# Performance work log

Hardware: AMD Instinct MI355X
Metric: run time of the kernel (lower is better)

The kernel has to match this reference:

```python
import jax, jax.numpy as jnp
import numpy as np

B, S, E, H = 2, 4096, 512, 8
DK = E // H


def setup_inputs() -> dict:
    k = jax.random.key(0)
    ks = jax.random.split(k, 11)
    sc = 0.02
    return {
        "query": jax.random.normal(ks[0], (B, S, E), jnp.float32),
        "key_in": jax.random.normal(ks[1], (B, S, E), jnp.float32),
        "value": jax.random.normal(ks[2], (B, S, E), jnp.float32),
        "Wq": jax.random.normal(ks[3], (E, E), jnp.float32) * sc,
        "bq": jax.random.normal(ks[4], (E,), jnp.float32) * sc,
        "Wk": jax.random.normal(ks[5], (E, E), jnp.float32) * sc,
        "bk": jax.random.normal(ks[6], (E,), jnp.float32) * sc,
        "Wv": jax.random.normal(ks[7], (E, E), jnp.float32) * sc,
        "bv": jax.random.normal(ks[8], (E,), jnp.float32) * sc,
        "Wo": jax.random.normal(ks[9], (E, E), jnp.float32) * sc,
        "bo": jax.random.normal(ks[10], (E,), jnp.float32) * sc,
    }


def reference(query, key_in, value, Wq, bq, Wk, bk, Wv, bv, Wo, bo):
    b, s, _ = query.shape
    # Linear projections
    q = query @ Wq + bq
    k = key_in @ Wk + bk
    v = value @ Wv + bv
    # [b, s, H, dk] -> [b, H, s, dk]
    q = q.reshape(b, s, H, DK).transpose(0, 2, 1, 3)
    k = k.reshape(b, s, H, DK).transpose(0, 2, 1, 3)
    v = v.reshape(b, s, H, DK).transpose(0, 2, 1, 3)
    # NOTE: source bug — softmax over UNSCALED scores (1/sqrt scaling in the
    # original is applied to a dead variable after softmax). Reproduce faithfully.
    scores = jnp.einsum("bhqd,bhkd->bhqk", q, k)  # [b,H,s,s] — O(N^2) materialized
    weights = jax.nn.softmax(scores.astype(jnp.float32), axis=-1)
    attn = jnp.einsum("bhqk,bhkd->bhqd", weights, v)
    # [b,H,s,dk] -> [b,s,E]
    concat = attn.transpose(0, 2, 1, 3).reshape(b, s, E)
    return concat @ Wo + bo
```

## Files before the change

### kernel.cpp

```cpp
#include <hip/hip_runtime.h>
#include <hip/hip_bf16.h>

#define B_  2
#define S_  4096
#define E_  512
#define H_  8
#define DK_ 64
#define M_  8192

typedef float f32x4  __attribute__((ext_vector_type(4)));
typedef float f32x16 __attribute__((ext_vector_type(16)));
typedef short s16x8  __attribute__((ext_vector_type(8)));
typedef short s16x4  __attribute__((ext_vector_type(4)));

static __device__ __forceinline__ short f2bf(float x) {
  __hip_bfloat16 h = __float2bfloat16(x);
  return __builtin_bit_cast(short, h);
}

static __device__ __forceinline__ f32x4 mfma32(s16x8 a, s16x8 b, f32x4 c) {
  return __builtin_amdgcn_mfma_f32_16x16x32_bf16(a, b, c, 0, 0, 0);
}

static __device__ __forceinline__ f32x16 mfma3232(s16x8 a, s16x8 b, f32x16 c) {
  return __builtin_amdgcn_mfma_f32_32x32x16_bf16(a, b, c, 0, 0, 0);
}

static __device__ __forceinline__ void gload_lds16(const void* g, void* l) {
  __builtin_amdgcn_global_load_lds(
      (const __attribute__((address_space(1))) unsigned int*)g,
      (__attribute__((address_space(3))) unsigned int*)l, 16, 0, 0);
}

static __device__ __forceinline__ int swz(int row, int colByte) {
  return row * 128 + (colByte ^ ((row & 7) << 4));
}

__global__ __launch_bounds__(256) void conv_bf16(const float* __restrict__ in,
                                                 short* __restrict__ out, int n4) {
  int i = blockIdx.x * 256 + threadIdx.x;
  if (i < n4) {
    float4 v = *((const float4*)in + i);
    s16x4 o;
    o[0] = f2bf(v.x); o[1] = f2bf(v.y); o[2] = f2bf(v.z); o[3] = f2bf(v.w);
    *((s16x4*)out + i) = o;
  }
}

__global__ __launch_bounds__(256) void conv_wT(const float* __restrict__ W,
                                               short* __restrict__ Wt) {
  int idx = blockIdx.x * 256 + threadIdx.x;
  int j = idx >> 9, k = idx & 511;
  Wt[idx] = f2bf(W[(size_t)k * E_ + j]);
}

static __device__ __forceinline__ void gemm_core_512(
    const short* __restrict__ A, const short* __restrict__ Bt,
    short* As, short* Bs, int tm, int tn, f32x4 acc[4][4]) {
  const int tid = threadIdx.x;
  const int wave = tid >> 6, lane = tid & 63;
  const int wm = (wave >> 1) * 64, wn = (wave & 1) * 64;
  const int c = lane & 15, g = lane >> 4;
  for (int kk = 0; kk < 512; kk += 64) {
#pragma unroll
    for (int i = 0; i < 4; ++i) {
      int ob = wave * 4096 + i * 1024 + lane * 16;
      int row = ob >> 7;
      int col = (ob & 127) >> 1;
      gload_lds16(A + (size_t)(tm + row) * 512 + kk + col,
                  (char*)As + wave * 4096 + i * 1024);
      gload_lds16(Bt + (size_t)(tn + row) * 512 + kk + col,
                  (char*)Bs + wave * 4096 + i * 1024);
    }
    __syncthreads();
#pragma unroll
    for (int s = 0; s < 2; ++s) {
      s16x8 af[4], bfr[4];
#pragma unroll
      for (int i = 0; i < 4; ++i)
        af[i] = *(const s16x8*)&As[(wm + i * 16 + c) * 64 + s * 32 + g * 8];
#pragma unroll
      for (int j = 0; j < 4; ++j)
        bfr[j] = *(const s16x8*)&Bs[(wn + j * 16 + c) * 64 + s * 32 + g * 8];
#pragma unroll
      for (int i = 0; i < 4; ++i)
#pragma unroll
        for (int j = 0; j < 4; ++j)
          acc[i][j] = mfma32(af[i], bfr[j], acc[i][j]);
    }
    __syncthreads();
  }
}

__global__ __launch_bounds__(256) void gemm_qkv(
    const short* __restrict__ Xq, const short* __restrict__ Xk,
    const short* __restrict__ Xv, const short* __restrict__ Wt,
    const float* __restrict__ bq, const float* __restrict__ bk,
    const float* __restrict__ bv,
    short* __restrict__ Qo, short* __restrict__ Ko, short* __restrict__ Vto) {
  __shared__ __align__(16) short As[128 * 64];
  __shared__ __align__(16) short Bs[128 * 64];
  const int z = blockIdx.z;
  const short* A = (z == 0) ? Xq : ((z == 1) ? Xk : Xv);
  const short* Bt = Wt + z * (E_ * E_);
  const float* bias = (z == 0) ? bq : ((z == 1) ? bk : bv);
  const int tm = blockIdx.x * 128, tn = blockIdx.y * 128;
  f32x4 acc[4][4] = {};
  gemm_core_512(A, Bt, As, Bs, tm, tn, acc);

  const int tid = threadIdx.x;
  const int wave = tid >> 6, lane = tid & 63;
  const int wm = (wave >> 1) * 64, wn = (wave & 1) * 64;
  const int c = lane & 15, g = lane >> 4;
#pragma unroll
  for (int i = 0; i < 4; ++i) {
#pragma unroll
    for (int j = 0; j < 4; ++j) {
      const int gc = tn + wn + j * 16 + c;
      const float bb = bias[gc];
      const int h = gc >> 6, dk = gc & 63;
#pragma unroll
      for (int r = 0; r < 4; ++r) {
        const int gr = tm + wm + i * 16 + g * 4 + r;
        const int b = gr >> 12, s = gr & 4095;
        const short hv = f2bf(acc[i][j][r] + bb);
        if (z == 2)
          Vto[(size_t)((b * H_ + h) * DK_ + dk) * S_ + s] = hv;
        else if (z == 1)
          Ko[(size_t)((b * H_ + h) * S_ + s) * DK_ + dk] = hv;
        else
          Qo[(size_t)((b * H_ + h) * S_ + s) * DK_ + dk] = hv;
      }
    }
  }
}

__global__ __launch_bounds__(256) void gemm_out(
    const short* __restrict__ AO, const short* __restrict__ Wot,
    const float* __restrict__ bo, float* __restrict__ out) {
  __shared__ __align__(16) short As[128 * 64];
  __shared__ __align__(16) short Bs[128 * 64];
  const int tm = blockIdx.x * 128, tn = blockIdx.y * 128;
  f32x4 acc[4][4] = {};
  gemm_core_512(AO, Wot, As, Bs, tm, tn, acc);

  const int tid = threadIdx.x;
  const int wave = tid >> 6, lane = tid & 63;
  const int wm = (wave >> 1) * 64, wn = (wave & 1) * 64;
  const int c = lane & 15, g = lane >> 4;
#pragma unroll
  for (int i = 0; i < 4; ++i) {
#pragma unroll
    for (int j = 0; j < 4; ++j) {
      const int gc = tn + wn + j * 16 + c;
      const float bb = bo[gc];
#pragma unroll
      for (int r = 0; r < 4; ++r) {
        const int gr = tm + wm + i * 16 + g * 4 + r;
        out[(size_t)gr * E_ + gc] = acc[i][j][r] + bb;
      }
    }
  }
}

__global__ __launch_bounds__(256, 2) void attn_fwd(
    const short* __restrict__ Q, const short* __restrict__ K,
    const short* __restrict__ Vt, short* __restrict__ O) {
  __shared__ __align__(16) short Ks[2][64 * 64];
  __shared__ __align__(16) short Vs[4][64 * 64];
  const int tid = threadIdx.x;
  const int wave = tid >> 6, lane = tid & 63;
  const int qi = lane & 31, hi = lane >> 5;
  const int bh = blockIdx.y;
  const int b = bh >> 3, h = bh & 7;
  const int q0 = blockIdx.x * 128 + wave * 32;
  const short* Qp = Q + (size_t)bh * S_ * DK_;
  const short* Kp = K + (size_t)bh * S_ * DK_;
  const short* Vp = Vt + (size_t)bh * DK_ * S_;

  s16x8 qf[4];
#pragma unroll
  for (int s = 0; s < 4; ++s)
    qf[s] = *(const s16x8*)(Qp + (size_t)(q0 + qi) * DK_ + s * 16 + hi * 8);

  f32x16 o0 = {}, o1 = {};
  f32x16 lacc = {};
  s16x8 ones;
#pragma unroll
  for (int e = 0; e < 8; ++e) ones[e] = (short)0x3F80;

  auto stageK = [&](int kt, int buf) {
#pragma unroll
    for (int r = 0; r < 2; ++r) {
      const int ob = wave * 2048 + r * 1024 + (lane << 4);
      const int row = ob >> 7;
      const int cbl = (ob & 127) ^ ((row & 7) << 4);
      const int srow = (row & 32) | ((row & 8) << 1) | ((row & 4) << 1) |
                       ((row & 16) >> 2) | (row & 3);
      gload_lds16(Kp + (size_t)(kt * 64 + srow) * DK_ + (cbl >> 1),
                  (char*)Ks[buf] + wave * 2048 + r * 1024);
    }
  };
  auto stageV = [&](int kt, int buf) {
#pragma unroll
    for (int r = 0; r < 2; ++r) {
      const int ob = wave * 2048 + r * 1024 + (lane << 4);
      const int row = ob >> 7;
      const int cbl = (ob & 127) ^ ((row & 7) << 4);
      gload_lds16(Vp + (size_t)row * S_ + kt * 64 + (cbl >> 1),
                  (char*)Vs[buf] + wave * 2048 + r * 1024);
    }
  };

  auto qk = [&](const short* Kbuf, f32x16& s0, f32x16& s1) {
    const char* Kc = (const char*)Kbuf;
    f32x16 t0 = {}, t1 = {};
#pragma unroll
    for (int s = 0; s < 4; ++s) {
      s16x8 ka = *(const s16x8*)(Kc + swz(qi, s * 32 + hi * 16));
      s16x8 kb = *(const s16x8*)(Kc + swz(32 + qi, s * 32 + hi * 16));
      t0 = mfma3232(ka, qf[s], t0);
      t1 = mfma3232(kb, qf[s], t1);
    }
    s0 = t0; s1 = t1;
  };

  auto softpv = [&](const f32x16& s0, const f32x16& s1, const short* Vbuf) {
    const char* Vc = (const char*)Vbuf;
    float p0[16], p1[16];
#pragma unroll
    for (int r = 0; r < 16; ++r) { p0[r] = __expf(s0[r]); p1[r] = __expf(s1[r]); }
    s16x8 pb[2][2];
#pragma unroll
    for (int ks = 0; ks < 2; ++ks)
#pragma unroll
      for (int j = 0; j < 8; ++j) {
        const int r = (j & 3) | (ks << 2) | ((j >> 2) << 3);
        pb[0][ks][j] = f2bf(p0[r]);
        pb[1][ks][j] = f2bf(p1[r]);
      }
    __builtin_amdgcn_s_setprio(1);
#pragma unroll
    for (int half = 0; half < 2; ++half)
#pragma unroll
      for (int ks = 0; ks < 2; ++ks) {
        s16x8 va0 = *(const s16x8*)(Vc + swz(qi, half * 64 + ks * 32 + hi * 16));
        s16x8 va1 = *(const s16x8*)(Vc + swz(32 + qi, half * 64 + ks * 32 + hi * 16));
        o0 = mfma3232(va0, pb[half][ks], o0);
        o1 = mfma3232(va1, pb[half][ks], o1);
        lacc = mfma3232(ones, pb[half][ks], lacc);
      }
    __builtin_amdgcn_s_setprio(0);
  };

  const int NT = S_ / 64;
  f32x16 sA0, sA1, sB0, sB1;

  stageK(0, 0); stageV(0, 0);
  __syncthreads();
  stageK(1, 1); stageV(1, 1);
  qk(Ks[0], sA0, sA1);
  __syncthreads();

  for (int t = 0; t < NT; t += 2) {
    if (t + 2 < NT) { stageK(t + 2, t & 1); stageV(t + 2, (t + 2) & 3); }
    qk(Ks[(t + 1) & 1], sB0, sB1);
    softpv(sA0, sA1, Vs[t & 3]);
    __syncthreads();
    if (t + 3 < NT) { stageK(t + 3, (t + 1) & 1); stageV(t + 3, (t + 3) & 3); }
    if (t + 2 < NT) qk(Ks[(t + 2) & 1], sA0, sA1);
    softpv(sB0, sB1, Vs[(t + 1) & 3]);
    __syncthreads();
  }

  const float rl = 1.f / lacc[0];
  short* Op = O + ((size_t)(b * S_ + q0 + qi)) * E_ + h * DK_;
#pragma unroll
  for (int rr = 0; rr < 4; ++rr) {
    s16x4 ov0, ov1;
#pragma unroll
    for (int e = 0; e < 4; ++e) {
      ov0[e] = f2bf(o0[rr * 4 + e] * rl);
      ov1[e] = f2bf(o1[rr * 4 + e] * rl);
    }
    *(s16x4*)(Op + rr * 8 + hi * 4) = ov0;
    *(s16x4*)(Op + 32 + rr * 8 + hi * 4) = ov1;
  }
}

extern "C" void kernel_launch(void* const* d_in, const int* in_sizes, int n_in,
                              void* d_out, int out_size, void* d_ws, size_t ws_size,
                              hipStream_t stream) {
  const float* query  = (const float*)d_in[0];
  const float* key_in = (const float*)d_in[1];
  const float* value  = (const float*)d_in[2];
  const float* Wq = (const float*)d_in[3];
  const float* bq = (const float*)d_in[4];
  const float* Wk = (const float*)d_in[5];
  const float* bk = (const float*)d_in[6];
  const float* Wv = (const float*)d_in[7];
  const float* bv = (const float*)d_in[8];
  const float* Wo = (const float*)d_in[9];
  const float* bo = (const float*)d_in[10];
  float* out = (float*)d_out;

  const size_t NA = (size_t)M_ * E_;
  short* ws  = (short*)d_ws;
  short* Xq  = ws;
  short* Xk  = Xq + NA;
  short* Xv  = Xk + NA;
  short* Wt  = Xv + NA;
  short* Wot = Wt + 3 * E_ * E_;
  short* Qb  = Wot + E_ * E_;
  short* Kb  = Qb + NA;
  short* Vtb = Kb + NA;
  short* AO  = Vtb + NA;

  conv_bf16<<<dim3(NA / 1024), 256, 0, stream>>>(query, Xq, (int)(NA / 4));
  conv_bf16<<<dim3(NA / 1024), 256, 0, stream>>>(key_in, Xk, (int)(NA / 4));
  conv_bf16<<<dim3(NA / 1024), 256, 0, stream>>>(value, Xv, (int)(NA / 4));
  conv_wT<<<dim3(E_ * E_ / 256), 256, 0, stream>>>(Wq, Wt);
  conv_wT<<<dim3(E_ * E_ / 256), 256, 0, stream>>>(Wk, Wt + E_ * E_);
  conv_wT<<<dim3(E_ * E_ / 256), 256, 0, stream>>>(Wv, Wt + 2 * E_ * E_);
  conv_wT<<<dim3(E_ * E_ / 256), 256, 0, stream>>>(Wo, Wot);

  gemm_qkv<<<dim3(M_ / 128, E_ / 128, 3), 256, 0, stream>>>(
      Xq, Xk, Xv, Wt, bq, bk, bv, Qb, Kb, Vtb);
  attn_fwd<<<dim3(S_ / 128, B_ * H_), 256, 0, stream>>>(Qb, Kb, Vtb, AO);
  gemm_out<<<dim3(M_ / 128, E_ / 128), 256, 0, stream>>>(AO, Wot, bo, out);
}
```

Before: 177.5 us.

## Split attention KV range across two wave groups and fold log2e into Q

The attention kernel now launches 512 threads per block. Two groups of four waves each process half of the key/value sequence, with per-group double-buffered K and triple-buffered V staging. The partial outputs and row sums are reduced through shared memory at the end. Q is pre-scaled by log2(e) in the projection epilogue so that softmax can use a hardware exp2. The two groups use different qk/softpv orderings to overlap MFMA and exp work, and setprio is added around QK. This doubles the waves per block to improve latency hiding, at the cost of extra reduction traffic and higher LDS use.

After: 266.0 us. 49.8% more time.

```diff
diff --git a/kernel.cpp b/kernel.cpp
--- a/kernel.cpp
+++ b/kernel.cpp
@@ -24,6 +24,14 @@
 
 static __device__ __forceinline__ f32x16 mfma3232(s16x8 a, s16x8 b, f32x16 c) {
   return __builtin_amdgcn_mfma_f32_32x32x16_bf16(a, b, c, 0, 0, 0);
+}
+
+static __device__ __forceinline__ float fastexp2(float x) {
+#if __has_builtin(__builtin_amdgcn_exp2f)
+  return __builtin_amdgcn_exp2f(x);
+#else
+  return __expf(x * 0.69314718056f);
+#endif
 }
 
 static __device__ __forceinline__ void gload_lds16(const void* g, void* l) {
@@ -123,7 +131,9 @@
       for (int r = 0; r < 4; ++r) {
         const int gr = tm + wm + i * 16 + g * 4 + r;
         const int b = gr >> 12, s = gr & 4095;
-        const short hv = f2bf(acc[i][j][r] + bb);
+        float v = acc[i][j][r] + bb;
+        if (z == 0) v *= 1.44269504f;
+        const short hv = f2bf(v);
         if (z == 2)
           Vto[(size_t)((b * H_ + h) * DK_ + dk) * S_ + s] = hv;
         else if (z == 1)
@@ -163,17 +173,19 @@
   }
 }
 
-__global__ __launch_bounds__(256, 2) void attn_fwd(
+__global__ __launch_bounds__(512, 4) void attn_fwd(
     const short* __restrict__ Q, const short* __restrict__ K,
     const short* __restrict__ Vt, short* __restrict__ O) {
-  __shared__ __align__(16) short Ks[2][64 * 64];
-  __shared__ __align__(16) short Vs[4][64 * 64];
+  __shared__ __align__(16) short Ks[2][2][64 * 64];
+  __shared__ __align__(16) short Vs[2][3][64 * 64];
   const int tid = threadIdx.x;
   const int wave = tid >> 6, lane = tid & 63;
+  const int wq = wave & 3, sid = wave >> 2;
   const int qi = lane & 31, hi = lane >> 5;
   const int bh = blockIdx.y;
   const int b = bh >> 3, h = bh & 7;
-  const int q0 = blockIdx.x * 128 + wave * 32;
+  const int q0 = blockIdx.x * 128 + wq * 32;
+  const int koff = sid * (S_ / 2);
   const short* Qp = Q + (size_t)bh * S_ * DK_;
   const short* Kp = K + (size_t)bh * S_ * DK_;
   const short* Vp = Vt + (size_t)bh * DK_ * S_;
@@ -189,32 +201,25 @@
 #pragma unroll
   for (int e = 0; e < 8; ++e) ones[e] = (short)0x3F80;
 
-  auto stageK = [&](int kt, int buf) {
+  auto stage = [&](int kt) {
 #pragma unroll
     for (int r = 0; r < 2; ++r) {
-      const int ob = wave * 2048 + r * 1024 + (lane << 4);
+      const int ob = wq * 2048 + r * 1024 + (lane << 4);
       const int row = ob >> 7;
       const int cbl = (ob & 127) ^ ((row & 7) << 4);
       const int srow = (row & 32) | ((row & 8) << 1) | ((row & 4) << 1) |
                        ((row & 16) >> 2) | (row & 3);
-      gload_lds16(Kp + (size_t)(kt * 64 + srow) * DK_ + (cbl >> 1),
-                  (char*)Ks[buf] + wave * 2048 + r * 1024);
-    }
-  };
-  auto stageV = [&](int kt, int buf) {
-#pragma unroll
-    for (int r = 0; r < 2; ++r) {
-      const int ob = wave * 2048 + r * 1024 + (lane << 4);
-      const int row = ob >> 7;
-      const int cbl = (ob & 127) ^ ((row & 7) << 4);
-      gload_lds16(Vp + (size_t)row * S_ + kt * 64 + (cbl >> 1),
-                  (char*)Vs[buf] + wave * 2048 + r * 1024);
+      gload_lds16(Kp + (size_t)(koff + kt * 64 + srow) * DK_ + (cbl >> 1),
+                  (char*)Ks[sid][kt & 1] + wq * 2048 + r * 1024);
+      gload_lds16(Vp + (size_t)row * S_ + koff + kt * 64 + (cbl >> 1),
+                  (char*)Vs[sid][kt % 3] + wq * 2048 + r * 1024);
     }
   };
 
   auto qk = [&](const short* Kbuf, f32x16& s0, f32x16& s1) {
     const char* Kc = (const char*)Kbuf;
     f32x16 t0 = {}, t1 = {};
+    __builtin_amdgcn_s_setprio(1);
 #pragma unroll
     for (int s = 0; s < 4; ++s) {
       s16x8 ka = *(const s16x8*)(Kc + swz(qi, s * 32 + hi * 16));
@@ -222,6 +227,7 @@
       t0 = mfma3232(ka, qf[s], t0);
       t1 = mfma3232(kb, qf[s], t1);
     }
+    __builtin_amdgcn_s_setprio(0);
     s0 = t0; s1 = t1;
   };
 
@@ -229,7 +235,7 @@
     const char* Vc = (const char*)Vbuf;
     float p0[16], p1[16];
 #pragma unroll
-    for (int r = 0; r < 16; ++r) { p0[r] = __expf(s0[r]); p1[r] = __expf(s1[r]); }
+    for (int r = 0; r < 16; ++r) { p0[r] = fastexp2(s0[r]); p1[r] = fastexp2(s1[r]); }
     s16x8 pb[2][2];
 #pragma unroll
     for (int ks = 0; ks < 2; ++ks)
@@ -253,38 +259,56 @@
     __builtin_amdgcn_s_setprio(0);
   };
 
-  const int NT = S_ / 64;
-  f32x16 sA0, sA1, sB0, sB1;
-
-  stageK(0, 0); stageV(0, 0);
+  const int NT2 = S_ / 2 / 64;
+  f32x16 sp0, sp1;
+
+  stage(0);
   __syncthreads();
-  stageK(1, 1); stageV(1, 1);
-  qk(Ks[0], sA0, sA1);
+
+  for (int t = 0; t < NT2; ++t) {
+    if (t + 1 < NT2) stage(t + 1);
+    if (sid == 0) {
+      f32x16 s0, s1;
+      qk(Ks[0][t & 1], s0, s1);
+      softpv(s0, s1, Vs[0][t % 3]);
+    } else {
+      if (t > 0) softpv(sp0, sp1, Vs[1][(t - 1) % 3]);
+      qk(Ks[1][t & 1], sp0, sp1);
+    }
+    __syncthreads();
+  }
+  if (sid == 1) softpv(sp0, sp1, Vs[1][(NT2 - 1) % 3]);
+
+  float* pO = (float*)Ks;
+  float* pL = (float*)Vs;
+  if (sid == 1) {
+#pragma unroll
+    for (int r = 0; r < 16; ++r) {
+      pO[r * 256 + wq * 64 + lane] = o0[r];
+      pO[(16 + r) * 256 + wq * 64 + lane] = o1[r];
+    }
+    pL[wq * 64 + lane] = lacc[0];
+  }
   __syncthreads();
-
-  for (int t = 0; t < NT; t += 2) {
-    if (t + 2 < NT) { stageK(t + 2, t & 1); stageV(t + 2, (t + 2) & 3); }
-    qk(Ks[(t + 1) & 1], sB0, sB1);
-    softpv(sA0, sA1, Vs[t & 3]);
-    __syncthreads();
-    if (t + 3 < NT) { stageK(t + 3, (t + 1) & 1); stageV(t + 3, (t + 3) & 3); }
-    if (t + 2 < NT) qk(Ks[(t + 2) & 1], sA0, sA1);
-    softpv(sB0, sB1, Vs[(t + 1) & 3]);
-    __syncthreads();
-  }
-
-  const float rl = 1.f / lacc[0];
-  short* Op = O + ((size_t)(b * S_ + q0 + qi)) * E_ + h * DK_;
-#pragma unroll
-  for (int rr = 0; rr < 4; ++rr) {
-    s16x4 ov0, ov1;
-#pragma unroll
-    for (int e = 0; e < 4; ++e) {
-      ov0[e] = f2bf(o0[rr * 4 + e] * rl);
-      ov1[e] = f2bf(o1[rr * 4 + e] * rl);
-    }
-    *(s16x4*)(Op + rr * 8 + hi * 4) = ov0;
-    *(s16x4*)(Op + 32 + rr * 8 + hi * 4) = ov1;
+  if (sid == 0) {
+#pragma unroll
+    for (int r = 0; r < 16; ++r) {
+      o0[r] += pO[r * 256 + wq * 64 + lane];
+      o1[r] += pO[(16 + r) * 256 + wq * 64 + lane];
+    }
+    const float rl = 1.f / (lacc[0] + pL[wq * 64 + lane]);
+    short* Op = O + ((size_t)(b * S_ + q0 + qi)) * E_ + h * DK_;
+#pragma unroll
+    for (int rr = 0; rr < 4; ++rr) {
+      s16x4 ov0, ov1;
+#pragma unroll
+      for (int e = 0; e < 4; ++e) {
+        ov0[e] = f2bf(o0[rr * 4 + e] * rl);
+        ov1[e] = f2bf(o1[rr * 4 + e] * rl);
+      }
+      *(s16x4*)(Op + rr * 8 + hi * 4) = ov0;
+      *(s16x4*)(Op + 32 + rr * 8 + hi * 4) = ov1;
+    }
   }
 }
 
@@ -326,6 +350,6 @@
 
   gemm_qkv<<<dim3(M_ / 128, E_ / 128, 3), 256, 0, stream>>>(
       Xq, Xk, Xv, Wt, bq, bk, bv, Qb, Kb, Vtb);
-  attn_fwd<<<dim3(S_ / 128, B_ * H_), 256, 0, stream>>>(Qb, Kb, Vtb, AO);
+  attn_fwd<<<dim3(S_ / 128, B_ * H_), 512, 0, stream>>>(Qb, Kb, Vtb, AO);
   gemm_out<<<dim3(M_ / 128, E_ / 128), 256, 0, stream>>>(AO, Wot, bo, out);
 }
```
